# Kernel optimization log

Measured on AMD Instinct MI355X. Metric: run time of the kernel, lower is better.

Reference implementation:

```python
import jax, jax.numpy as jnp
import numpy as np
from jax import lax
from jax.scipy.special import gammaln

B, T_FEATS, T_TEXT = 16, 2000, 400
ADIM, ODIM = 256, 512
BIG_NEG = -1e30
BLANK_LOGP = -1.0  # log(blank_prob) with blank_prob = e**-1


def _conv1d(x, w, b, pad):
    # x: (B, C_in, L), w: (C_out, C_in, K)
    y = lax.conv_general_dilated(x, w, (1,), [(pad, pad)],
                                 dimension_numbers=('NCH', 'OIH', 'NCH'))
    return y + b[None, :, None]


def _betabinom_prior(T, N):
    # ESPnet AlignmentModule beta-binomial attention prior (w=1):
    # alpha_t = t (1..T), beta_t = T - t + 1, k = 1..N, n = N
    t = jnp.arange(1, T + 1, dtype=jnp.float32)
    a = t[:, None]                                   # (T,1)
    bb = (T - t + 1.0)[:, None]                      # (T,1)
    k = jnp.arange(1, N + 1, dtype=jnp.float32)[None, :]  # (1,N)
    n = float(N)
    betaln = lambda x, y: gammaln(x) + gammaln(y) - gammaln(x + y)
    logC = gammaln(n + 1.0) - gammaln(k + 1.0) - gammaln(n - k + 1.0)
    return logC + betaln(k + a, n - k + bb) - betaln(a, bb)  # (T,N)


def _alignment_encoder(txt, speech, tw1, tb1, tw2, tb2, fw1, fb1, fw2, fb2, fw3, fb3):
    t = txt.transpose(0, 2, 1)                       # (B, adim, T_text)
    t = jax.nn.relu(_conv1d(t, tw1, tb1, 1))
    t = _conv1d(t, tw2, tb2, 0)
    t = t.transpose(0, 2, 1)                         # (B, T_text, adim)

    f = speech.transpose(0, 2, 1)                    # (B, odim, T_feats)
    f = jax.nn.relu(_conv1d(f, fw1, fb1, 1))
    f = jax.nn.relu(_conv1d(f, fw2, fb2, 1))
    f = _conv1d(f, fw3, fb3, 0)
    f = f.transpose(0, 2, 1)                         # (B, T_feats, adim)

    # score = -||f_t - t_s||_2 via expansion (avoids (B,T,S,D) intermediate)
    d2 = (jnp.sum(f * f, -1)[:, :, None] + jnp.sum(t * t, -1)[:, None, :]
          - 2.0 * jnp.einsum('btd,bsd->bts', f, t))
    score = -jnp.sqrt(jnp.maximum(d2, 1e-12))        # (B, T_feats, T_text)
    logp = jax.nn.log_softmax(score, axis=-1)
    return logp + _betabinom_prior(T_FEATS, T_TEXT)[None]


def _forwardsum_loss(log_p_attn):
    # CTC forward algorithm; targets are 1..N (all distinct) + interleaved blanks
    Bv, T, N = log_p_attn.shape
    lp = jnp.concatenate(
        [jnp.full((Bv, T, 1), BLANK_LOGP, log_p_attn.dtype), log_p_attn], axis=-1)
    lp = jax.nn.log_softmax(lp, axis=-1)             # (B, T, N+1)
    S = 2 * N + 1
    ext = np.zeros(S, np.int32); ext[1::2] = np.arange(1, N + 1)
    skip_ok = np.zeros(S, bool); skip_ok[3::2] = True  # non-blank, distinct labels
    ext = jnp.asarray(ext); skip_ok = jnp.asarray(skip_ok)

    emit = lp[:, :, ext]                             # (B, T, S)
    alpha = jnp.full((Bv, S), BIG_NEG)
    alpha = alpha.at[:, 0].set(emit[:, 0, 0]).at[:, 1].set(emit[:, 0, 1])

    def step(alpha, e):
        a1 = jnp.concatenate([jnp.full((Bv, 1), BIG_NEG), alpha[:, :-1]], axis=1)
        a2 = jnp.concatenate([jnp.full((Bv, 2), BIG_NEG), alpha[:, :-2]], axis=1)
        a2 = jnp.where(skip_ok[None, :], a2, BIG_NEG)
        alpha = jnp.logaddexp(jnp.logaddexp(alpha, a1), a2) + e
        return alpha, None

    alpha, _ = lax.scan(step, alpha, jnp.moveaxis(emit[:, 1:], 1, 0))
    nll = -jnp.logaddexp(alpha[:, -1], alpha[:, -2])  # (B,)
    # F.ctc_loss reduction='mean' divides each sample's nll by target length
    return jnp.mean(nll / N)


def _mas_single(lp):
    # lp: (T_feats, T_text) -> monotonic alignment (T_feats,) int32
    log_prob = lp.T                                  # (N, T)
    N, T = T_TEXT, T_FEATS
    q0 = jnp.where(jnp.arange(N) == 0, log_prob[0, 0], BIG_NEG)

    def fwd(q, col):
        q = jnp.maximum(q, jnp.concatenate([jnp.full((1,), BIG_NEG), q[:-1]])) + col
        return q, q

    _, qs = lax.scan(fwd, q0, log_prob[:, 1:].T)     # (T-1, N)
    Q = lax.stop_gradient(jnp.concatenate([q0[None], qs], axis=0))  # (T, N)

    def bwd(a_next, q_col):
        i_a = jnp.maximum(a_next - 1, 0)
        a = jnp.where(a_next == 0, 0,
                      jnp.where(q_col[i_a] >= q_col[a_next], i_a, a_next))
        a = a.astype(jnp.int32)
        return a, a

    _, A_rev = lax.scan(bwd, jnp.array(N - 1, jnp.int32), Q[:-1], reverse=True)
    return jnp.concatenate([A_rev, jnp.array([N - 1], jnp.int32)])  # (T,)


def _viterbi_decode(log_p_attn):
    A = jax.vmap(_mas_single)(log_p_attn)            # (B, T_feats) int32
    ds = jax.vmap(lambda a: jnp.bincount(a, length=T_TEXT))(A)
    ds = ds.astype(log_p_attn.dtype)                 # (B, T_text) durations
    gathered = jnp.take_along_axis(log_p_attn, A[:, :, None], axis=2)[..., 0]
    bin_loss = -jnp.mean(jnp.mean(gathered, axis=1))
    return ds, bin_loss


def setup_inputs() -> dict:
    key = jax.random.key(0)
    ks = jax.random.split(key, 12)
    s = 0.05
    inp = {
        'speech': jax.random.normal(ks[0], (B, T_FEATS, ODIM), jnp.float32),
        'txt': jax.random.normal(ks[1], (B, T_TEXT, ADIM), jnp.float32),
        'speech_len': jnp.full((B,), T_FEATS, jnp.int32),
        'txt_len': jnp.full((B,), T_TEXT, jnp.int32),
        'tw1': jax.random.normal(ks[2], (ADIM, ADIM, 3)) * s,
        'tb1': jnp.zeros((ADIM,)),
        'tw2': jax.random.normal(ks[3], (ADIM, ADIM, 1)) * s,
        'tb2': jnp.zeros((ADIM,)),
        'fw1': jax.random.normal(ks[4], (ADIM, ODIM, 3)) * s,
        'fb1': jnp.zeros((ADIM,)),
        'fw2': jax.random.normal(ks[5], (ADIM, ADIM, 3)) * s,
        'fb2': jnp.zeros((ADIM,)),
        'fw3': jax.random.normal(ks[6], (ADIM, ADIM, 1)) * s,
        'fb3': jnp.zeros((ADIM,)),
    }
    return inp


def reference(speech, txt, speech_len, txt_len,
              tw1, tb1, tw2, tb2, fw1, fb1, fw2, fb2, fw3, fb3):
    # lengths are full (no padding), so masks are no-ops
    log_p_attn = _alignment_encoder(txt, speech, tw1, tb1, tw2, tb2,
                                    fw1, fb1, fw2, fb2, fw3, fb3)
    forwardsum_loss = _forwardsum_loss(log_p_attn)
    ds, bin_loss = _viterbi_decode(log_p_attn)
    return ds, bin_loss, forwardsum_loss, log_p_attn
```

## Files before the change

### kernel.cpp

```cpp
#include <hip/hip_runtime.h>
#include <math.h>

typedef unsigned int u32;
typedef unsigned long long u64;
typedef unsigned short u16;
typedef __attribute__((ext_vector_type(8))) _Float16 f16x8;
typedef __attribute__((ext_vector_type(4))) float f32x4;

#define BIGN (-1e30f)

static constexpr int NB = 16;
static constexpr int TF = 2000;
static constexpr int TT = 400;

__device__ __forceinline__ float wsum(float v){
#pragma unroll
  for(int o=32;o;o>>=1) v += __shfl_xor(v,o,64);
  return v;
}
__device__ __forceinline__ float EXP2(float x){ return __builtin_amdgcn_exp2f(x); }
__device__ __forceinline__ float LOG2(float x){ return __builtin_amdgcn_logf(x); }
__device__ __forceinline__ float lse2b(float x, float y){
  float m = fmaxf(x,y);
  return m + LOG2(1.0f + EXP2(-fabsf(x-y)));
}
__device__ __forceinline__ float lse3b(float x, float y, float z){
  float mx = fmaxf(fmaxf(x,y),z);
  float md = __builtin_amdgcn_fmed3f(x,y,z);
  float mn = fminf(fminf(x,y),z);
  return mx + LOG2(1.0f + EXP2(md-mx) + EXP2(mn-mx));
}
__device__ __forceinline__ u16 f2h(float v){
  _Float16 h = (_Float16)v;
  return *(u16*)&h;
}
__device__ __forceinline__ float shup1(float v){
  int r = __builtin_amdgcn_update_dpp(__float_as_int(BIGN), __float_as_int(v),
                                      0x138, 0xf, 0xf, false);
  return __int_as_float(r);
}

__global__ void k_lgt(double* lgt){
  int m = blockIdx.x*blockDim.x + threadIdx.x;
  if(m < 2432) lgt[m] = (m>=1)? lgamma((double)m) : 0.0;
}
__global__ void k_terms(const double* __restrict__ lgt, double* rowA, double* colA, double* sA){
  int i = blockIdx.x*blockDim.x + threadIdx.x;
  if(i < TF)   rowA[i] = -lgt[2401] - lgt[i+1] - lgt[2000-i] + lgt[2001];
  if(i < TT)   colA[i] =  lgt[401]  - lgt[i+2] - lgt[400-i];
  if(i < 2399) sA[i]   =  lgt[i+2]  + lgt[2399-i];
}

__device__ __forceinline__ void packf(const float* __restrict__ w, u16* __restrict__ dst,
    int CIN, int KW, int i){
  int k = i % KW;
  int c = (i / KW) % CIN;
  int o = i / (KW*CIN);
  dst[((size_t)k*256 + o)*CIN + c] = f2h(w[i]);
}
__device__ __forceinline__ void cvtp(const float* __restrict__ src, u16* __restrict__ dst,
    int P, int C, int i){
  int c = i % C;
  int p = (i / C) % (P+2);
  int b = i / (C*(P+2));
  float v = 0.f;
  if(p>=1 && p<=P) v = src[((size_t)b*P + (p-1))*C + c];
  dst[i] = f2h(v);
}
__device__ __forceinline__ void zpr(u16* __restrict__ buf, int P, int j){
  int c = j % 256;
  int s = (j / 256) & 1;
  int b = j / 512;
  buf[((size_t)b*(P+2) + (s? P+1 : 0))*256 + c] = 0;
}
__global__ __launch_bounds__(256) void prep1_k(
    const float* __restrict__ fw1, const float* __restrict__ fw2, const float* __restrict__ fw3,
    const float* __restrict__ tw1, const float* __restrict__ tw2, const float* __restrict__ txt,
    u16* fw1p, u16* fw2p, u16* fw3p, u16* tw1p, u16* tw2p,
    u16* inbfT, u16* tout1, u16* out1){
  constexpr int N = 393216+196608+65536+196608+65536+1646592+8192+8192;
  for(int i = blockIdx.x*256 + threadIdx.x; i < N; i += gridDim.x*256){
    int j = i;
    if(j < 393216){ packf(fw1, fw1p, 512, 3, j); continue; } j -= 393216;
    if(j < 196608){ packf(fw2, fw2p, 256, 3, j); continue; } j -= 196608;
    if(j < 65536) { packf(fw3, fw3p, 256, 1, j); continue; } j -= 65536;
    if(j < 196608){ packf(tw1, tw1p, 256, 3, j); continue; } j -= 196608;
    if(j < 65536) { packf(tw2, tw2p, 256, 1, j); continue; } j -= 65536;
    if(j < 1646592){ cvtp(txt, inbfT, TT, 256, j); continue; } j -= 1646592;
    if(j < 8192) { zpr(tout1, TT, j); continue; } j -= 8192;
    zpr(out1, TF, j);
  }
}

__global__ __launch_bounds__(256) void cvt_pad_k(const float* __restrict__ src, u16* __restrict__ dst,
    int P, int C){
  int n = NB*(P+2)*C;
  for(int i = blockIdx.x*256 + threadIdx.x; i < n; i += gridDim.x*256) cvtp(src, dst, P, C, i);
}
__global__ __launch_bounds__(256) void zpad_k(u16* __restrict__ buf, int P){
  int n = NB*2*256;
  for(int i = blockIdx.x*256 + threadIdx.x; i < n; i += gridDim.x*256) zpr(buf, P, i);
}

template<int CIN, int KW, bool RELU, bool OBF>
__global__ __launch_bounds__(256) void mfconv_k(const u16* __restrict__ inb,
    const u16* __restrict__ wp, const float* __restrict__ bias, void* __restrict__ outp, int P){
  __shared__ __align__(16) u16 Al[4*66*8];
  __shared__ __align__(16) u16 Bl[KW*4*256*8];
  const int b = blockIdx.y;
  const int m0 = blockIdx.x * 64;
  const int tid = threadIdx.x;
  const int lane = tid & 63, wv = tid >> 6;
  const int lo16 = lane & 15, hi = lane >> 4;
  constexpr int K1 = (KW==1)? 1 : 0;
  const u16* inB = inb + (size_t)b*(P+2)*CIN;
  f32x4 acc[4][4];
#pragma unroll
  for(int i=0;i<4;i++)
#pragma unroll
    for(int j=0;j<4;j++) acc[i][j] = (f32x4){0.f,0.f,0.f,0.f};

  for(int c0=0; c0<CIN; c0+=32){
    __syncthreads();
    for(int idx = tid; idx < 264; idx += 256){
      int r = idx >> 2, q = idx & 3;
      int rowp = m0 + r;
      f16x8 v = (f16x8){0,0,0,0,0,0,0,0};
      if(rowp <= P+1) v = *(const f16x8*)&inB[(size_t)rowp*CIN + c0 + q*8];
      *(f16x8*)&Al[(q*66 + r)*8] = v;
    }
#pragma unroll
    for(int k=0;k<KW;k++){
      const u16* wr = &wp[((size_t)(k*256) + tid)*CIN + c0];
      f16x8 w0 = *(const f16x8*)&wr[0];
      f16x8 w1 = *(const f16x8*)&wr[8];
      f16x8 w2 = *(const f16x8*)&wr[16];
      f16x8 w3 = *(const f16x8*)&wr[24];
      *(f16x8*)&Bl[((k*4+0)*256 + tid)*8] = w0;
      *(f16x8*)&Bl[((k*4+1)*256 + tid)*8] = w1;
      *(f16x8*)&Bl[((k*4+2)*256 + tid)*8] = w2;
      *(f16x8*)&Bl[((k*4+3)*256 + tid)*8] = w3;
    }
    __syncthreads();
#pragma unroll
    for(int k=0;k<KW;k++){
      f16x8 af[4];
#pragma unroll
      for(int rf=0;rf<4;rf++)
        af[rf] = *(const f16x8*)&Al[(hi*66 + rf*16 + lo16 + k + K1)*8];
#pragma unroll
      for(int cf=0;cf<4;cf++){
        int o = wv*64 + cf*16 + lo16;
        f16x8 bf = *(const f16x8*)&Bl[((k*4+hi)*256 + o)*8];
#pragma unroll
        for(int rf=0;rf<4;rf++)
          acc[rf][cf] = __builtin_amdgcn_mfma_f32_16x16x32_f16(af[rf], bf, acc[rf][cf], 0, 0, 0);
      }
    }
  }
#pragma unroll
  for(int cf=0;cf<4;cf++){
    int o = wv*64 + cf*16 + lo16;
    float bs = bias[o];
#pragma unroll
    for(int rf=0;rf<4;rf++){
#pragma unroll
      for(int j=0;j<4;j++){
        int p = m0 + rf*16 + hi*4 + j;
        if(p < P){
          float v = acc[rf][cf][j] + bs;
          if(RELU) v = fmaxf(v, 0.f);
          if(OBF) ((u16*)outp)[((size_t)b*(P+2) + p + 1)*256 + o] = f2h(v);
          else    ((float*)outp)[((size_t)b*P + p)*256 + o] = v;
        }
      }
    }
  }
}

__global__ __launch_bounds__(256) void norm2b_k(const float* __restrict__ x1, const float* __restrict__ x2,
    float* __restrict__ o1, float* __restrict__ o2){
  int r = blockIdx.x*4 + (threadIdx.x>>6);
  int lane = threadIdx.x & 63;
  const float* src; float* dst; int rr;
  if(r < NB*TF){ src = x1; dst = o1; rr = r; }
  else { rr = r - NB*TF; if(rr >= NB*TT) return; src = x2; dst = o2; }
  float4 v = ((const float4*)(src + (size_t)rr*256))[lane];
  float s = v.x*v.x + v.y*v.y + v.z*v.z + v.w*v.w;
  s = wsum(s);
  if(lane==0) dst[rr] = s;
}

__global__ __launch_bounds__(256) void score_gemm(const float* __restrict__ F, const float* __restrict__ Tn,
    const float* __restrict__ fn2, const float* __restrict__ tn2, float* __restrict__ outp){
  constexpr int KC = 32;
  __shared__ __align__(16) float As[KC][68];
  __shared__ __align__(16) float Bs[KC][68];
  const int b = blockIdx.z;
  const int t0 = blockIdx.y*64, s0 = blockIdx.x*64;
  const int tid = threadIdx.x, tx = tid&15, ty = tid>>4;
  const float* Fb = F  + (size_t)b*TF*256;
  const float* Tb = Tn + (size_t)b*TT*256;
  float acc[4][4] = {};
  const int lk = tid & 31, lt0 = (tid>>5)*8;
  for(int k0=0;k0<256;k0+=KC){
    __syncthreads();
#pragma unroll
    for(int i=0;i<8;i++){
      int t = t0 + lt0 + i;
      As[lk][lt0+i] = (t<TF)? Fb[(size_t)t*256 + k0 + lk] : 0.f;
      int s = s0 + lt0 + i;
      Bs[lk][lt0+i] = (s<TT)? Tb[(size_t)s*256 + k0 + lk] : 0.f;
    }
    __syncthreads();
#pragma unroll
    for(int k=0;k<KC;k++){
      float a0[4], b0[4];
      *(float4*)a0 = *(const float4*)&As[k][ty*4];
      *(float4*)b0 = *(const float4*)&Bs[k][tx*4];
#pragma unroll
      for(int i=0;i<4;i++)
#pragma unroll
        for(int j=0;j<4;j++) acc[i][j] = fmaf(a0[i], b0[j], acc[i][j]);
    }
  }
#pragma unroll
  for(int i=0;i<4;i++){
    int t = t0 + ty*4 + i;
    if(t<TF){
      float fn = fn2[b*TF + t];
#pragma unroll
      for(int j=0;j<4;j++){
        int s = s0 + tx*4 + j;
        if(s<TT){
          float d2 = fn + tn2[b*TT + s] - 2.f*acc[i][j];
          outp[((size_t)b*TF + t)*TT + s] = -sqrtf(fmaxf(d2, 1e-12f));
        }
      }
    }
  }
}

__global__ __launch_bounds__(128) void softmax_prior_k(float* __restrict__ logp,
    const double* __restrict__ rowA, const double* __restrict__ colA, const double* __restrict__ sA,
    float* __restrict__ Z2){
  const int row = blockIdx.x;
  const int t0 = row % TF;
  float* rp = logp + (size_t)row*TT;
  const int tid = threadIdx.x;
  __shared__ float sh2[2];
  float v[4]; int ix[4];
#pragma unroll
  for(int i=0;i<4;i++){ ix[i] = tid + i*128; v[i] = (ix[i]<TT)? rp[ix[i]] : BIGN; }
  float m = fmaxf(fmaxf(v[0],v[1]),fmaxf(v[2],v[3]));
#pragma unroll
  for(int o=32;o;o>>=1) m = fmaxf(m, __shfl_xor(m,o,64));
  if((tid&63)==0) sh2[tid>>6] = m;
  __syncthreads();
  m = fmaxf(sh2[0], sh2[1]);
  float s = 0.f;
#pragma unroll
  for(int i=0;i<4;i++) if(ix[i]<TT) s += __expf(v[i]-m);
  s = wsum(s);
  __syncthreads();
  if((tid&63)==0) sh2[tid>>6] = s;
  __syncthreads();
  s = sh2[0] + sh2[1];
  const float lse = m + __logf(s);
  const double rA = rowA[t0];
  float f[4]; float m2 = BIGN;
#pragma unroll
  for(int i=0;i<4;i++){
    if(ix[i]<TT){
      float pr = (float)(colA[ix[i]] + sA[t0+ix[i]] + rA);
      f[i] = (v[i]-lse) + pr;
      rp[ix[i]] = f[i];
      m2 = fmaxf(m2, f[i]);
    } else f[i] = BIGN;
  }
#pragma unroll
  for(int o=32;o;o>>=1) m2 = fmaxf(m2, __shfl_xor(m2,o,64));
  __syncthreads();
  if((tid&63)==0) sh2[tid>>6] = m2;
  __syncthreads();
  m2 = fmaxf(fmaxf(sh2[0],sh2[1]), -1.0f);
  float s2 = (tid==0)? __expf(-1.0f - m2) : 0.f;
#pragma unroll
  for(int i=0;i<4;i++) if(ix[i]<TT) s2 += __expf(f[i]-m2);
  s2 = wsum(s2);
  __syncthreads();
  if((tid&63)==0) sh2[tid>>6] = s2;
  __syncthreads();
  if(tid==0) Z2[row] = m2 + __logf(sh2[0]+sh2[1]);
}

#define LCTC4(E) { \
  float n1 = shup1(a[3]); \
  float t1 = lse3b(a[1], a[0], n1)   + (E)[0]; \
  float t3 = lse3b(a[3], a[2], a[1]) + (E)[1]; \
  float t0 = lse2b(a[0], n1)   + EBL; \
  float t2 = lse2b(a[2], a[1]) + EBL; \
  a[0]=t0; a[1]=t1; a[2]=t2; a[3]=t3; }

#define CPREF2(E, K) { int kk=(K); if(kk>999) kk=999; int row = dir? (TF-1-kk) : kk; \
  const float* rpp = lp + (size_t)row*TT; \
  (E)[0]=rpp[jc0]*IL2; (E)[1]=rpp[jc1]*IL2; }

#define SEAMW(BUF) if(q<3 && lane>=wl0 && lane<wl0+4){ \
  float* sp = &sb[dir][q][BUF][(lane-wl0)*4]; \
  sp[0]=a[0]; sp[1]=a[1]; sp[2]=a[2]; sp[3]=a[3]; }

#define HALOR(BUF) if(q>0 && lane<4){ \
  const float* sp = &sb[dir][q-1][BUF][lane*4]; \
  a[0]=sp[0]; a[1]=sp[1]; a[2]=sp[2]; a[3]=sp[3]; }

#define MAS_STEP(E, TIDX) { \
  float n1 = shup1(q[6]); \
  u32 byte = 0; \
  if(lane>0 && n1 >= q[0]) byte |= 1u; \
  if(q[0] >= q[1]) byte |= 2u; \
  if(q[1] >= q[2]) byte |= 4u; \
  if(q[2] >= q[3]) byte |= 8u; \
  if(q[3] >= q[4]) byte |= 16u; \
  if(q[4] >= q[5]) byte |= 32u; \
  if(q[5] >= q[6]) byte |= 64u; \
  cb[(size_t)((TIDX)-1)*64 + lane] = (unsigned char)byte; \
  q[6] = fmaxf(q[6], q[5]) + (E)[6]; \
  q[5] = fmaxf(q[5], q[4]) + (E)[5]; \
  q[4] = fmaxf(q[4], q[3]) + (E)[4]; \
  q[3] = fmaxf(q[3], q[2]) + (E)[3]; \
  q[2] = fmaxf(q[2], q[1]) + (E)[2]; \
  q[1] = fmaxf(q[1], q[0]) + (E)[1]; \
  q[0] = fmaxf(q[0], n1) + (E)[0]; }

#define MPREF(E, ROW) { int rr=(ROW); rr = (rr>TF-1)? (TF-1) : rr; const float* rpp = lp + (size_t)rr*TT; \
  (E)[0]=rpp[jc[0]]; (E)[1]=rpp[jc[1]]; (E)[2]=rpp[jc[2]]; (E)[3]=rpp[jc[3]]; \
  (E)[4]=rpp[jc[4]]; (E)[5]=rpp[jc[5]]; (E)[6]=rpp[jc[6]]; }

__global__ __launch_bounds__(512) __attribute__((amdgpu_waves_per_eu(2,2)))
void scan_k(const float* __restrict__ logp,
    const float* __restrict__ Z2, unsigned char* __restrict__ cmpb, float* __restrict__ nll){
  const int lane = threadIdx.x & 63;
  const int wave = threadIdx.x >> 6;
  constexpr float IL2 = 1.4426950408889634f;
  constexpr float L2  = 0.6931471805599453f;
  if(blockIdx.x < NB){
    const int b = blockIdx.x;
    const float* lp = logp + (size_t)b*TF*TT;
    __shared__ float af[801], ag[801];
    __shared__ float sb[2][3][2][16];
    const int dir = wave >> 2;
    const int q   = wave & 3;
    const int sbase = (q==0)? 0 : 200*q - 16;
    const int olo = 200*q;
    const int ohi = (q<3)? 200*q+199 : 800;
    const int wl0 = (q==0)? 46 : 50;
    double zs = 0.0;
    if(wave==0){
      for(int t=lane; t<TF; t+=64) zs += (double)Z2[b*TF + t];
#pragma unroll
      for(int o=32;o;o>>=1) zs += __shfl_xor(zs, o, 64);
    }
    int j0 = sbase/2 + 2*lane, j1 = j0 + 1;
    if(dir){ j0 = TT-1-j0; j1 = TT-1-j1; }
    const int jc0 = (j0<0)? 0 : ((j0>TT-1)? TT-1 : j0);
    const int jc1 = (j1<0)? 0 : ((j1>TT-1)? TT-1 : j1);
    float a[4];
#pragma unroll
    for(int i=0;i<4;i++) a[i] = BIGN;
    if(q==0 && lane==0){
      a[0] = -1.0f*IL2;
      a[1] = (dir? lp[(size_t)(TF-1)*TT + (TT-1)] : lp[0]) * IL2;
    }
    const float EBL = -1.0f*IL2;
    SEAMW(0);
    float e0[2],e1[2],e2[2],e3[2],e4[2],e5[2],e6[2],e7[2];
    CPREF2(e0,1); CPREF2(e1,2); CPREF2(e2,3); CPREF2(e3,4);
    CPREF2(e4,5); CPREF2(e5,6); CPREF2(e6,7); CPREF2(e7,8);
    __syncthreads();
    int k = 1, kb = 0;
    for(; k + 8 <= 1000; k += 8, kb++){
      HALOR(kb&1);
      LCTC4(e0); CPREF2(e0, k+8);
      LCTC4(e1); CPREF2(e1, k+9);
      LCTC4(e2); CPREF2(e2, k+10);
      LCTC4(e3); CPREF2(e3, k+11);
      LCTC4(e4); CPREF2(e4, k+12);
      LCTC4(e5); CPREF2(e5, k+13);
      LCTC4(e6); CPREF2(e6, k+14);
      LCTC4(e7); CPREF2(e7, k+15);
      SEAMW((kb+1)&1);
      __syncthreads();
    }
    HALOR(kb&1);
    for(; k<=999; k++){
      float P[2];
      CPREF2(P, k);
      LCTC4(P);
    }
    float* dst = dir? ag : af;
#pragma unroll
    for(int i=0;i<4;i++){
      int s = sbase + 4*lane + i;
      if(s>=olo && s<=ohi) dst[s] = a[i];
    }
    __syncthreads();
    if(wave==0){
      float acc = BIGN;
      for(int s = lane; s <= 800; s += 64){
        float x0 = af[s];
        float x1 = (s>=1)? af[s-1] : BIGN;
        float x2 = ((s&1) && s>=3)? af[s-2] : BIGN;
        float A1 = lse3b(x0,x1,x2);
        acc = lse2b(acc, A1 + ag[800-s]);
      }
#pragma unroll
      for(int o=32;o;o>>=1) acc = lse2b(acc, __shfl_xor(acc,o,64));
      if(lane==0) nll[b] = -((acc*L2) - (float)zs);
    }
  } else {
    if(wave) return;
    const int b = blockIdx.x - NB;
    const float* lp = logp + (size_t)b*TF*TT;
    unsigned char* cb = cmpb + (size_t)b*TF*64;
    int jc[7];
#pragma unroll
    for(int i=0;i<7;i++){ int j = 7*lane + i; jc[i] = (j < TT)? j : (TT-1); }
    float q[7];
#pragma unroll
    for(int i=0;i<7;i++) q[i] = BIGN;
    if(lane==0) q[0] = lp[0];
    float e0[7],e1[7],e2[7],e3[7];
    MPREF(e0,1); MPREF(e1,2); MPREF(e2,3); MPREF(e3,4);
    int t0 = 1;
    for(; t0 + 4 <= TF; t0 += 4){
      MAS_STEP(e0, t0);   MPREF(e0, t0+4);
      MAS_STEP(e1, t0+1); MPREF(e1, t0+5);
      MAS_STEP(e2, t0+2); MPREF(e2, t0+6);
      MAS_STEP(e3, t0+3); MPREF(e3, t0+7);
    }
    for(; t0<TF; t0++){
      float P[7];
      MPREF(P, t0);
      MAS_STEP(P, t0);
    }
    {
      float n1 = shup1(q[6]);
      u32 byte = 0;
      if(lane>0 && n1 >= q[0]) byte |= 1u;
      if(q[0] >= q[1]) byte |= 2u;
      if(q[1] >= q[2]) byte |= 4u;
      if(q[2] >= q[3]) byte |= 8u;
      if(q[3] >= q[4]) byte |= 16u;
      if(q[4] >= q[5]) byte |= 32u;
      if(q[5] >= q[6]) byte |= 64u;
      cb[(size_t)(TF-1)*64 + lane] = (unsigned char)byte;
    }
  }
}

__global__ __launch_bounds__(256) void masback_k(const unsigned char* __restrict__ cmpb,
    const float* __restrict__ logp, float* __restrict__ ds, float* __restrict__ gsum){
  const int b = blockIdx.x;
  const unsigned char* cb = cmpb + (size_t)b*TF*64;
  __shared__ unsigned char bits[500*64];
  __shared__ short Ash[TF];
  __shared__ int cnt[TT];
  __shared__ float ps[4];
  int a = TT-1;
  for(int ch=3; ch>=0; ch--){
    const int tlo = ch*500;
    __syncthreads();
    for(int i=threadIdx.x;i<8000;i+=256) ((u32*)bits)[i] = ((const u32*)(cb + (size_t)tlo*64))[i];
    __syncthreads();
    if(threadIdx.x==0){
      int thi = tlo + 499;
      if(ch==3){ Ash[TF-1] = (short)(TT-1); thi = TF-2; }
      for(int t=thi;t>=tlo;t--){
        if(a > 0){
          unsigned char w = bits[(t-tlo)*64 + a/7];
          a -= (int)((w >> (a%7)) & 1u);
        }
        Ash[t] = (short)a;
      }
    }
  }
  __syncthreads();
  for(int i=threadIdx.x;i<TT;i+=256) cnt[i]=0;
  __syncthreads();
  float part = 0.f;
  const float* lp = logp + (size_t)b*TF*TT;
  for(int t=threadIdx.x;t<TF;t+=256){
    int at = Ash[t];
    atomicAdd(&cnt[at], 1);
    part += lp[(size_t)t*TT + at];
  }
  __syncthreads();
  for(int i=threadIdx.x;i<TT;i+=256) ds[(size_t)b*TT + i] = (float)cnt[i];
  part = wsum(part);
  if((threadIdx.x&63)==0) ps[threadIdx.x>>6] = part;
  __syncthreads();
  if(threadIdx.x==0) gsum[b] = ps[0]+ps[1]+ps[2]+ps[3];
}

__global__ void final_k(const float* __restrict__ nll, const float* __restrict__ gsum, float* __restrict__ out){
  if(threadIdx.x==0 && blockIdx.x==0){
    float fs=0.f, bs=0.f;
    for(int b=0;b<NB;b++){ fs += nll[b] / (float)TT; bs += gsum[b] / (float)TF; }
    out[6400] = -(bs / (float)NB);
    out[6401] = fs / (float)NB;
  }
}

extern "C" void kernel_launch(void* const* d_in, const int* in_sizes, int n_in,
                              void* d_out, int out_size, void* d_ws, size_t ws_size,
                              hipStream_t stream){
  const float* speech = (const float*)d_in[0];
  const float* txt    = (const float*)d_in[1];
  const float* tw1 = (const float*)d_in[4];
  const float* tb1 = (const float*)d_in[5];
  const float* tw2 = (const float*)d_in[6];
  const float* tb2 = (const float*)d_in[7];
  const float* fw1 = (const float*)d_in[8];
  const float* fb1 = (const float*)d_in[9];
  const float* fw2 = (const float*)d_in[10];
  const float* fb2 = (const float*)d_in[11];
  const float* fw3 = (const float*)d_in[12];
  const float* fb3 = (const float*)d_in[13];
  float* out  = (float*)d_out;
  float* ds   = out;
  float* logp = out + 6402;
  char* ws = (char*)d_ws;
  double* lgt  = (double*)(ws + 0);
  double* rowA = (double*)(ws + 20480);
  double* colA = (double*)(ws + 36864);
  double* sA   = (double*)(ws + 40960);
  float*  nll  = (float*)(ws + 61440);
  float*  gsum = (float*)(ws + 61696);
  float*  Z2   = (float*)(ws + 65536);
  float*  fn2  = (float*)(ws + 196608);
  float*  tn2  = (float*)(ws + 327680);
  unsigned char* cmpb = (unsigned char*)(ws + 360448);
  float*  tenc = (float*)(ws + 2408448);
  float*  f1   = (float*)(ws + 8962048);
  if(ws_size < 41730048) return;

  char* lr = (char*)(((uintptr_t)logp + 255) & ~(uintptr_t)255);
  u16* inbfT = (u16*)lr;
  u16* tout1 = (u16*)(lr + 4000000);
  u16* inbfA = (u16*)lr;
  u16* out2  = (u16*)lr;
  u16* wbase = (u16*)(lr + 32900000);
  u16* fw1p = wbase;
  u16* fw2p = wbase + 393216;
  u16* fw3p = wbase + 589824;
  u16* tw1p = wbase + 655360;
  u16* tw2p = wbase + 851968;
  u16* out1  = (u16*)(lr + 34750000);

  k_lgt  <<<10,256,0,stream>>>(lgt);
  k_terms<<<10,256,0,stream>>>(lgt,rowA,colA,sA);

  prep1_k<<<2048,256,0,stream>>>(fw1,fw2,fw3,tw1,tw2, txt,
                                 fw1p,fw2p,fw3p,tw1p,tw2p, inbfT, tout1, out1);

  mfconv_k<256,3,true ,true ><<<dim3(7,NB),256,0,stream>>>(inbfT, tw1p, tb1, tout1, TT);
  mfconv_k<256,1,false,false><<<dim3(7,NB),256,0,stream>>>(tout1, tw2p, tb2, tenc, TT);

  cvt_pad_k<<<4096,256,0,stream>>>(speech, inbfA, TF, 512);
  mfconv_k<512,3,true ,true ><<<dim3(32,NB),256,0,stream>>>(inbfA, fw1p, fb1, out1, TF);
  zpad_k<<<32,256,0,stream>>>(out2, TF);
  mfconv_k<256,3,true ,true ><<<dim3(32,NB),256,0,stream>>>(out1, fw2p, fb2, out2, TF);
  mfconv_k<256,1,false,false><<<dim3(32,NB),256,0,stream>>>(out2, fw3p, fb3, f1, TF);

  norm2b_k<<<(NB*TF+NB*TT)/4,256,0,stream>>>(f1, tenc, fn2, tn2);

  score_gemm<<<dim3(7,32,NB),256,0,stream>>>(f1, tenc, fn2, tn2, logp);
  softmax_prior_k<<<NB*TF,128,0,stream>>>(logp, rowA, colA, sA, Z2);

  scan_k<<<2*NB,512,0,stream>>>(logp, Z2, cmpb, nll);
  masback_k<<<NB,256,0,stream>>>(cmpb, logp, ds, gsum);
  final_k<<<1,64,0,stream>>>(nll, gsum, out);
}
```

Baseline: 818.4 us.

## Compute distance score GEMM with fp16 MFMA and store encoder outputs as fp16

The final conv layers now write fp16 instead of fp32 outputs. The fp32 FMA score GEMM is replaced by an MFMA 16x16x32 f16 kernel that reads these fp16 encodings, and the squared-norm kernel also reads fp16. This cuts memory traffic and moves the distance matmul onto matrix cores. The cost is lower precision in the distances, and with the expansion form d2 = |f|^2 + |t|^2 - 2f·t that loss can show up as cancellation error.

```diff
diff --git a/kernel.cpp b/kernel.cpp
--- a/kernel.cpp
+++ b/kernel.cpp
@@ -5,6 +5,7 @@
 typedef unsigned long long u64;
 typedef unsigned short u16;
 typedef __attribute__((ext_vector_type(8))) _Float16 f16x8;
+typedef __attribute__((ext_vector_type(4))) _Float16 f16x4;
 typedef __attribute__((ext_vector_type(4))) float f32x4;
 
 #define BIGN (-1e30f)
@@ -102,7 +103,7 @@
   for(int i = blockIdx.x*256 + threadIdx.x; i < n; i += gridDim.x*256) zpr(buf, P, i);
 }
 
-template<int CIN, int KW, bool RELU, bool OBF>
+template<int CIN, int KW, bool RELU, int OM>
 __global__ __launch_bounds__(256) void mfconv_k(const u16* __restrict__ inb,
     const u16* __restrict__ wp, const float* __restrict__ bias, void* __restrict__ outp, int P){
   __shared__ __align__(16) u16 Al[4*66*8];
@@ -170,72 +171,74 @@
         if(p < P){
           float v = acc[rf][cf][j] + bs;
           if(RELU) v = fmaxf(v, 0.f);
-          if(OBF) ((u16*)outp)[((size_t)b*(P+2) + p + 1)*256 + o] = f2h(v);
-          else    ((float*)outp)[((size_t)b*P + p)*256 + o] = v;
+          if(OM==1)      ((u16*)outp)[((size_t)b*(P+2) + p + 1)*256 + o] = f2h(v);
+          else if(OM==2) ((u16*)outp)[((size_t)b*P + p)*256 + o] = f2h(v);
+          else           ((float*)outp)[((size_t)b*P + p)*256 + o] = v;
         }
       }
     }
   }
 }
 
-__global__ __launch_bounds__(256) void norm2b_k(const float* __restrict__ x1, const float* __restrict__ x2,
+__global__ __launch_bounds__(256) void norm2h_k(const u16* __restrict__ fh, const u16* __restrict__ th,
     float* __restrict__ o1, float* __restrict__ o2){
   int r = blockIdx.x*4 + (threadIdx.x>>6);
   int lane = threadIdx.x & 63;
-  const float* src; float* dst; int rr;
-  if(r < NB*TF){ src = x1; dst = o1; rr = r; }
-  else { rr = r - NB*TF; if(rr >= NB*TT) return; src = x2; dst = o2; }
-  float4 v = ((const float4*)(src + (size_t)rr*256))[lane];
-  float s = v.x*v.x + v.y*v.y + v.z*v.z + v.w*v.w;
+  const u16* src; float* dst; int rr;
+  if(r < NB*TF){ src = fh; dst = o1; rr = r; }
+  else { rr = r - NB*TF; if(rr >= NB*TT) return; src = th; dst = o2; }
+  f16x4 v = *(const f16x4*)&src[(size_t)rr*256 + lane*4];
+  float x0=(float)v[0], x1=(float)v[1], x2=(float)v[2], x3=(float)v[3];
+  float s = x0*x0 + x1*x1 + x2*x2 + x3*x3;
   s = wsum(s);
   if(lane==0) dst[rr] = s;
 }
 
-__global__ __launch_bounds__(256) void score_gemm(const float* __restrict__ F, const float* __restrict__ Tn,
+__global__ __launch_bounds__(256) void score_mf(const u16* __restrict__ fh, const u16* __restrict__ th,
     const float* __restrict__ fn2, const float* __restrict__ tn2, float* __restrict__ outp){
-  constexpr int KC = 32;
-  __shared__ __align__(16) float As[KC][68];
-  __shared__ __align__(16) float Bs[KC][68];
+  __shared__ __align__(16) u16 Fl[4*64*8];
+  __shared__ __align__(16) u16 Tl[4*64*8];
   const int b = blockIdx.z;
-  const int t0 = blockIdx.y*64, s0 = blockIdx.x*64;
-  const int tid = threadIdx.x, tx = tid&15, ty = tid>>4;
-  const float* Fb = F  + (size_t)b*TF*256;
-  const float* Tb = Tn + (size_t)b*TT*256;
-  float acc[4][4] = {};
-  const int lk = tid & 31, lt0 = (tid>>5)*8;
-  for(int k0=0;k0<256;k0+=KC){
-    __syncthreads();
-#pragma unroll
-    for(int i=0;i<8;i++){
-      int t = t0 + lt0 + i;
-      As[lk][lt0+i] = (t<TF)? Fb[(size_t)t*256 + k0 + lk] : 0.f;
-      int s = s0 + lt0 + i;
-      Bs[lk][lt0+i] = (s<TT)? Tb[(size_t)s*256 + k0 + lk] : 0.f;
-    }
-    __syncthreads();
-#pragma unroll
-    for(int k=0;k<KC;k++){
-      float a0[4], b0[4];
-      *(float4*)a0 = *(const float4*)&As[k][ty*4];
-      *(float4*)b0 = *(const float4*)&Bs[k][tx*4];
-#pragma unroll
-      for(int i=0;i<4;i++)
-#pragma unroll
-        for(int j=0;j<4;j++) acc[i][j] = fmaf(a0[i], b0[j], acc[i][j]);
-    }
-  }
-#pragma unroll
-  for(int i=0;i<4;i++){
-    int t = t0 + ty*4 + i;
-    if(t<TF){
-      float fn = fn2[b*TF + t];
-#pragma unroll
-      for(int j=0;j<4;j++){
-        int s = s0 + tx*4 + j;
-        if(s<TT){
-          float d2 = fn + tn2[b*TT + s] - 2.f*acc[i][j];
-          outp[((size_t)b*TF + t)*TT + s] = -sqrtf(fmaxf(d2, 1e-12f));
-        }
+  const int t0 = blockIdx.y*64;
+  const int s0 = blockIdx.x*64;
+  const int tid = threadIdx.x;
+  const int lane = tid & 63, wv = tid >> 6;
+  const int lo16 = lane & 15, hi = lane >> 4;
+  const u16* fB = fh + (size_t)b*TF*256;
+  const u16* tB = th + (size_t)b*TT*256;
+  f32x4 acc[4];
+#pragma unroll
+  for(int c=0;c<4;c++) acc[c] = (f32x4){0.f,0.f,0.f,0.f};
+  const int srow = tid >> 2, sq = tid & 3;
+  for(int k0=0;k0<256;k0+=32){
+    __syncthreads();
+    {
+      f16x8 fv = (f16x8){0,0,0,0,0,0,0,0};
+      int fr = t0 + srow;
+      if(fr < TF) fv = *(const f16x8*)&fB[(size_t)fr*256 + k0 + sq*8];
+      *(f16x8*)&Fl[(sq*64 + srow)*8] = fv;
+      f16x8 tv = (f16x8){0,0,0,0,0,0,0,0};
+      int tr = s0 + srow;
+      if(tr < TT) tv = *(const f16x8*)&tB[(size_t)tr*256 + k0 + sq*8];
+      *(f16x8*)&Tl[(sq*64 + srow)*8] = tv;
+    }
+    __syncthreads();
+    f16x8 af = *(const f16x8*)&Fl[(hi*64 + wv*16 + lo16)*8];
+#pragma unroll
+    for(int cf=0;cf<4;cf++){
+      f16x8 bf = *(const f16x8*)&Tl[(hi*64 + cf*16 + lo16)*8];
+      acc[cf] = __builtin_amdgcn_mfma_f32_16x16x32_f16(af, bf, acc[cf], 0, 0, 0);
+    }
+  }
+#pragma unroll
+  for(int cf=0;cf<4;cf++){
+    int s = s0 + cf*16 + lo16;
+#pragma unroll
+    for(int j=0;j<4;j++){
+      int f = t0 + wv*16 + hi*4 + j;
+      if(f < TF && s < TT){
+        float d2 = fn2[b*TF + f] + tn2[b*TT + s] - 2.f*acc[cf][j];
+        outp[((size_t)b*TF + f)*TT + s] = -sqrtf(fmaxf(d2, 1e-12f));
       }
     }
   }
@@ -541,8 +544,8 @@
   float*  fn2  = (float*)(ws + 196608);
   float*  tn2  = (float*)(ws + 327680);
   unsigned char* cmpb = (unsigned char*)(ws + 360448);
-  float*  tenc = (float*)(ws + 2408448);
-  float*  f1   = (float*)(ws + 8962048);
+  u16*    th   = (u16*)(ws + 2408448);
+  u16*    fh   = (u16*)(ws + 8962048);
   if(ws_size < 41730048) return;
 
   char* lr = (char*)(((uintptr_t)logp + 255) & ~(uintptr_t)255);
@@ -564,18 +567,18 @@
   prep1_k<<<2048,256,0,stream>>>(fw1,fw2,fw3,tw1,tw2, txt,
                                  fw1p,fw2p,fw3p,tw1p,tw2p, inbfT, tout1, out1);
 
-  mfconv_k<256,3,true ,true ><<<dim3(7,NB),256,0,stream>>>(inbfT, tw1p, tb1, tout1, TT);
-  mfconv_k<256,1,false,false><<<dim3(7,NB),256,0,stream>>>(tout1, tw2p, tb2, tenc, TT);
+  mfconv_k<256,3,true ,1><<<dim3(7,NB),256,0,stream>>>(inbfT, tw1p, tb1, tout1, TT);
+  mfconv_k<256,1,false,2><<<dim3(7,NB),256,0,stream>>>(tout1, tw2p, tb2, th, TT);
 
   cvt_pad_k<<<4096,256,0,stream>>>(speech, inbfA, TF, 512);
-  mfconv_k<512,3,true ,true ><<<dim3(32,NB),256,0,stream>>>(inbfA, fw1p, fb1, out1, TF);
+  mfconv_k<512,3,true ,1><<<dim3(32,NB),256,0,stream>>>(inbfA, fw1p, fb1, out1, TF);
   zpad_k<<<32,256,0,stream>>>(out2, TF);
-  mfconv_k<256,3,true ,true ><<<dim3(32,NB),256,0,stream>>>(out1, fw2p, fb2, out2, TF);
-  mfconv_k<256,1,false,false><<<dim3(32,NB),256,0,stream>>>(out2, fw3p, fb3, f1, TF);
-
-  norm2b_k<<<(NB*TF+NB*TT)/4,256,0,stream>>>(f1, tenc, fn2, tn2);
-
-  score_gemm<<<dim3(7,32,NB),256,0,stream>>>(f1, tenc, fn2, tn2, logp);
+  mfconv_k<256,3,true ,1><<<dim3(32,NB),256,0,stream>>>(out1, fw2p, fb2, out2, TF);
+  mfconv_k<256,1,false,2><<<dim3(32,NB),256,0,stream>>>(out2, fw3p, fb3, fh, TF);
+
+  norm2h_k<<<(NB*TF+NB*TT)/4,256,0,stream>>>(fh, th, fn2, tn2);
+
+  score_mf<<<dim3(7,32,NB),256,0,stream>>>(fh, th, fn2, tn2, logp);
   softmax_prior_k<<<NB*TF,128,0,stream>>>(logp, rowA, colA, sA, Z2);
 
   scan_k<<<2*NB,512,0,stream>>>(logp, Z2, cmpb, nll);
```

Measured after the change: 730.0 us. 10.8% less time.
